# Optimization experiments

Measured on AMD Instinct MI355X. Metric: run time of the kernel, lower is better.

Reference implementation:

```python
import jax, jax.numpy as jnp
import numpy as np

V_MIN = -10.0
V_MAX = 10.0
NUM_ATOMS = 251
B = 131072
N_OBS = 128
N_ACT = 32
HID = 512


def _ln(x, g, b, eps=1e-5):
    m = jnp.mean(x, axis=-1, keepdims=True)
    v = jnp.var(x, axis=-1, keepdims=True)
    return (x - m) * jax.lax.rsqrt(v + eps) * g + b


def setup_inputs() -> dict:
    key = jax.random.key(0)
    ks = jax.random.split(key, 16)

    def lin(k, fi, fo):
        kw, kb = jax.random.split(k)
        lim = 1.0 / np.sqrt(fi)
        W = jax.random.uniform(kw, (fi, fo), jnp.float32, -lim, lim)
        b = jax.random.uniform(kb, (fo,), jnp.float32, -lim, lim)
        return W, b

    W1, b1 = lin(ks[0], N_OBS + N_ACT, HID)
    W2, b2 = lin(ks[1], HID, HID // 2)
    W3, b3 = lin(ks[2], HID // 2, HID // 4)
    W4, b4 = lin(ks[3], HID // 4, NUM_ATOMS)

    return {
        "obs": jax.random.normal(ks[4], (B, N_OBS), jnp.float32),
        "actions": jax.random.normal(ks[5], (B, N_ACT), jnp.float32),
        "rewards": jax.random.normal(ks[6], (B,), jnp.float32),
        "bootstrap": (jax.random.uniform(ks[7], (B,)) > 0.05).astype(jnp.float32),
        "discount": jnp.full((B,), 0.99, jnp.float32),
        "q_support": jnp.linspace(V_MIN, V_MAX, NUM_ATOMS, dtype=jnp.float32),
        "W1": W1, "b1": b1, "g1": jnp.ones((HID,), jnp.float32), "be1": jnp.zeros((HID,), jnp.float32),
        "W2": W2, "b2": b2, "g2": jnp.ones((HID // 2,), jnp.float32), "be2": jnp.zeros((HID // 2,), jnp.float32),
        "W3": W3, "b3": b3, "g3": jnp.ones((HID // 4,), jnp.float32), "be3": jnp.zeros((HID // 4,), jnp.float32),
        "W4": W4, "b4": b4,
    }


def _net(obs, actions, W1, b1, g1, be1, W2, b2, g2, be2, W3, b3, g3, be3, W4, b4):
    x = jnp.concatenate([obs, actions], axis=1)
    x = jax.nn.silu(_ln(x @ W1 + b1, g1, be1))
    x = jax.nn.silu(_ln(x @ W2 + b2, g2, be2))
    x = jax.nn.silu(_ln(x @ W3 + b3, g3, be3))
    return x @ W4 + b4  # [B, NUM_ATOMS] logits


def reference(obs, actions, rewards, bootstrap, discount, q_support,
              W1, b1, g1, be1, W2, b2, g2, be2, W3, b3, g3, be3, W4, b4):
    # C51 categorical projection (DistributionalQNetwork.projection)
    delta_z = (V_MAX - V_MIN) / (NUM_ATOMS - 1)
    bsz = rewards.shape[0]
    target_z = rewards[:, None] + bootstrap[:, None] * discount[:, None] * q_support[None, :]
    target_z = jnp.clip(target_z, V_MIN, V_MAX)
    b = (target_z - V_MIN) / delta_z  # fractional bin positions [B, A]
    lower = jnp.floor(b).astype(jnp.int32)
    upper = jnp.ceil(b).astype(jnp.int32)
    is_integer = upper == lower
    lower_mask = (lower > 0) & is_integer
    upper_mask = (lower == 0) & is_integer
    lower = jnp.where(lower_mask, lower - 1, lower)
    upper = jnp.where(upper_mask, upper + 1, upper)

    logits = _net(obs, actions, W1, b1, g1, be1, W2, b2, g2, be2, W3, b3, g3, be3, W4, b4)
    next_dist = jax.nn.softmax(logits, axis=1)

    offset = (jnp.arange(bsz, dtype=jnp.int32) * NUM_ATOMS)[:, None]  # [B,1]
    max_index = bsz * NUM_ATOMS - 1
    li = jnp.clip((lower + offset).reshape(-1), 0, max_index)
    ui = jnp.clip((upper + offset).reshape(-1), 0, max_index)

    w_lo = (next_dist * (upper.astype(jnp.float32) - b)).reshape(-1)
    w_hi = (next_dist * (b - lower.astype(jnp.float32))).reshape(-1)

    proj = jnp.zeros((bsz * NUM_ATOMS,), next_dist.dtype)
    proj = proj.at[li].add(w_lo).at[ui].add(w_hi)
    return proj.reshape(bsz, NUM_ATOMS)
```

## Files before the change

### kernel.cpp

```cpp
#include <hip/hip_runtime.h>


#define THREADS 256
#define PREP_THREADS 256

typedef __attribute__((ext_vector_type(8))) short short8v;
typedef __attribute__((ext_vector_type(4))) float f32x4;

__device__ __forceinline__ unsigned short f2bf(float f) {
  union { float f; unsigned u; } v; v.f = f;
  unsigned u = v.u;
  u += 0x7fffu + ((u >> 16) & 1u);
  return (unsigned short)(u >> 16);
}
__device__ __forceinline__ unsigned pack2bf(float a, float b) {
  return (unsigned)f2bf(a) | ((unsigned)f2bf(b) << 16);
}

__global__ void prep_kernel(const float* __restrict__ W1, const float* __restrict__ W2,
                            const float* __restrict__ W3, const float* __restrict__ W4,
                            unsigned short* __restrict__ ws) {
  int i = blockIdx.x * PREP_THREADS + threadIdx.x;
  if (i < 81920) {
    int n = i / 160, k = i - n * 160;
    ws[i] = f2bf(W1[k * 512 + n]);
  } else if (i < 212992) {
    int j = i - 81920; int n = j >> 9, k = j & 511;
    ws[i] = f2bf(W2[k * 256 + n]);
  } else if (i < 245760) {
    int j = i - 212992; int n = j >> 8, k = j & 255;
    ws[i] = f2bf(W3[k * 128 + n]);
  } else if (i < 278528) {
    int j = i - 245760; int n = j >> 7, k = j & 127;
    ws[i] = (n < 251) ? f2bf(W4[k * 251 + n]) : (unsigned short)0;
  }
}

#define OFF_R   0
#define OFF_ZS  32768
#define OFF_B4  33792
#define OFF_RED 34816
#define LDS_TOTAL 36096

template<int KD, int NFT>
__device__ __forceinline__ void gemm_w(const unsigned short* __restrict__ WT,
                                       const unsigned char* __restrict__ Hb,
                                       int fbase, f32x4 (&acc)[NFT][2]) {
  const int lane = threadIdx.x & 63;
  const int lm = lane & 15, kg = lane >> 4;
  constexpr int KS  = KD / 32;
  constexpr int G   = (NFT > 4) ? 2 : 1;
  constexpr int FPG = NFT / G;
  constexpr int NIT = KS * G;

  int woff[NFT];
#pragma unroll
  for (int ft = 0; ft < NFT; ++ft)
    woff[ft] = (fbase + ft * 16 + lm) * KD + kg * 8;

  int boff[2][2];
#pragma unroll
  for (int rt = 0; rt < 2; ++rt) {
    const int r = rt * 16 + lm;
    const int swz = (r & 7) << 4;
    const int base = r * (KD * 2) + kg * 16;
    boff[rt][0] = base ^ swz;
    boff[rt][1] = (base + 64) ^ swz;
  }

  short8v abuf[2][FPG];
  short8v bbuf[2][2];
#pragma unroll
  for (int rt = 0; rt < 2; ++rt)
    bbuf[0][rt] = *(const short8v*)(Hb + boff[rt][0]);
#pragma unroll
  for (int f = 0; f < FPG; ++f)
    abuf[0][f] = *(const short8v*)(WT + woff[f]);

#pragma unroll
  for (int it = 0; it < NIT; ++it) {
    const int ks = it / G, g = it % G;
    const int cur = it & 1, nxt = cur ^ 1;
    if (it + 1 < NIT) {
      const int nit = it + 1;
      const int nks = nit / G, ng = nit % G;
      if (ng == 0) {
        const int koff = (nks >> 1) * 128;
#pragma unroll
        for (int rt = 0; rt < 2; ++rt)
          bbuf[nks & 1][rt] = *(const short8v*)(Hb + boff[rt][nks & 1] + koff);
      }
#pragma unroll
      for (int f = 0; f < FPG; ++f)
        abuf[nxt][f] = *(const short8v*)(WT + woff[ng * FPG + f] + nks * 32);
    }
#pragma unroll
    for (int f = 0; f < FPG; ++f) {
      const int ft = g * FPG + f;
      acc[ft][0] = __builtin_amdgcn_mfma_f32_16x16x32_bf16(abuf[cur][f], bbuf[ks & 1][0], acc[ft][0], 0, 0, 0);
      acc[ft][1] = __builtin_amdgcn_mfma_f32_16x16x32_bf16(abuf[cur][f], bbuf[ks & 1][1], acc[ft][1], 0, 0, 0);
    }
  }
}

template<int ND, int NFT>
__device__ __forceinline__ void ln_silu_store(
    f32x4 (&acc)[NFT][2],
    const float* __restrict__ bias, const float* __restrict__ g,
    const float* __restrict__ be, unsigned char* __restrict__ Hb,
    float* __restrict__ redL, int fbase, int fq)
{
  const int lane = threadIdx.x & 63;
  const int lm = lane & 15, kg = lane >> 4;
  float s[2] = {0.f, 0.f}, q[2] = {0.f, 0.f};
#pragma unroll
  for (int ft = 0; ft < NFT; ++ft) {
    const int f0 = fbase + ft * 16 + kg * 4;
    const f32x4 bb = *(const f32x4*)(bias + f0);
#pragma unroll
    for (int rt = 0; rt < 2; ++rt)
#pragma unroll
      for (int rg = 0; rg < 4; ++rg) {
        float x = acc[ft][rt][rg] + bb[rg];
        acc[ft][rt][rg] = x;
        s[rt] += x; q[rt] += x * x;
      }
  }
#pragma unroll
  for (int rt = 0; rt < 2; ++rt) {
    s[rt] += __shfl_xor(s[rt], 16); s[rt] += __shfl_xor(s[rt], 32);
    q[rt] += __shfl_xor(q[rt], 16); q[rt] += __shfl_xor(q[rt], 32);
  }
  if (lane < 16) {
#pragma unroll
    for (int rt = 0; rt < 2; ++rt) {
      redL[(rt * 16 + lm) * 9 + fq * 2    ] = s[rt];
      redL[(rt * 16 + lm) * 9 + fq * 2 + 1] = q[rt];
    }
  }
  __syncthreads();
  float mean[2], rstd[2];
#pragma unroll
  for (int rt = 0; rt < 2; ++rt) {
    const int row = rt * 16 + lm;
    float S = 0.f, Q = 0.f;
#pragma unroll
    for (int w = 0; w < 4; ++w) {
      S += redL[row * 9 + w * 2];
      Q += redL[row * 9 + w * 2 + 1];
    }
    float m = S * (1.0f / ND);
    float v = Q * (1.0f / ND) - m * m;
    mean[rt] = m; rstd[rt] = rsqrtf(v + 1e-5f);
  }
#pragma unroll
  for (int ft = 0; ft < NFT; ++ft) {
    const int f0 = fbase + ft * 16 + kg * 4;
    const f32x4 g4 = *(const f32x4*)(g + f0);
    const f32x4 e4 = *(const f32x4*)(be + f0);
#pragma unroll
    for (int rt = 0; rt < 2; ++rt) {
      const int row = rt * 16 + lm;
      float h[4];
#pragma unroll
      for (int rg = 0; rg < 4; ++rg) {
        float y = (acc[ft][rt][rg] - mean[rt]) * rstd[rt] * g4[rg] + e4[rg];
        h[rg] = y * (1.0f / (1.0f + __expf(-y)));
      }
      uint2 w; w.x = pack2bf(h[0], h[1]); w.y = pack2bf(h[2], h[3]);
      int byte = row * (ND * 2) + f0 * 2;
      byte ^= ((row & 7) << 4);
      *(uint2*)(Hb + byte) = w;
    }
  }
}

__global__ __launch_bounds__(THREADS, 4) void fused_kernel(
    const float* __restrict__ obs, const float* __restrict__ actions,
    const float* __restrict__ rewards, const float* __restrict__ bootstrap,
    const float* __restrict__ discount, const float* __restrict__ q_support,
    const float* __restrict__ b1, const float* __restrict__ g1, const float* __restrict__ be1,
    const float* __restrict__ b2, const float* __restrict__ g2, const float* __restrict__ be2,
    const float* __restrict__ b3, const float* __restrict__ g3, const float* __restrict__ be3,
    const float* __restrict__ b4,
    const unsigned short* __restrict__ ws,
    float* __restrict__ out)
{
  __shared__ __align__(16) unsigned char smem[LDS_TOTAL];
  const int tid  = threadIdx.x;
  const int fq   = tid >> 6;
  const int lane = tid & 63;
  const int lm   = lane & 15;
  const int kg   = lane >> 4;
  const int row0 = blockIdx.x * 32;

  const unsigned short* W1T = ws;
  const unsigned short* W2T = ws + 81920;
  const unsigned short* W3T = ws + 212992;
  const unsigned short* W4T = ws + 245760;

  float* zsL  = (float*)(smem + OFF_ZS);
  float* b4L  = (float*)(smem + OFF_B4);
  float* redL = (float*)(smem + OFF_RED);

  float rw[2], bt[2], dc[2];
#pragma unroll
  for (int rt = 0; rt < 2; ++rt) {
    const int r = row0 + rt * 16 + lm;
    rw[rt] = rewards[r]; bt[rt] = bootstrap[r]; dc[rt] = discount[r];
  }

  zsL[tid] = (tid < 251) ? q_support[tid] : 0.f;
  b4L[tid] = (tid < 251) ? b4[tid] : 0.f;

  {
    unsigned char* Xb = smem + OFF_R;
#pragma unroll
    for (int it = 0; it < 5; ++it) {
      const int qq = it * THREADS + tid;
      const int r  = qq / 40;
      const int c4 = (qq - r * 40) * 4;
      float4 v;
      if (c4 < 128) v = *(const float4*)(obs + (size_t)(row0 + r) * 128 + c4);
      else          v = *(const float4*)(actions + (size_t)(row0 + r) * 32 + (c4 - 128));
      uint2 w; w.x = pack2bf(v.x, v.y); w.y = pack2bf(v.z, v.w);
      int byte = r * 320 + c4 * 2;
      byte ^= ((r & 7) << 4);
      *(uint2*)(Xb + byte) = w;
    }
  }
  __syncthreads();

  f32x4 acc1[8][2];
#pragma unroll
  for (int i = 0; i < 8; ++i) { acc1[i][0] = f32x4{0,0,0,0}; acc1[i][1] = f32x4{0,0,0,0}; }
  gemm_w<160, 8>(W1T, smem + OFF_R, fq * 128, acc1);
  ln_silu_store<512, 8>(acc1, b1, g1, be1, smem + OFF_R, redL, fq * 128, fq);
  __syncthreads();

  f32x4 acc2[4][2];
#pragma unroll
  for (int i = 0; i < 4; ++i) { acc2[i][0] = f32x4{0,0,0,0}; acc2[i][1] = f32x4{0,0,0,0}; }
  gemm_w<512, 4>(W2T, smem + OFF_R, fq * 64, acc2);
  ln_silu_store<256, 4>(acc2, b2, g2, be2, smem + OFF_R, redL, fq * 64, fq);
  __syncthreads();

  f32x4 acc3[2][2];
#pragma unroll
  for (int i = 0; i < 2; ++i) { acc3[i][0] = f32x4{0,0,0,0}; acc3[i][1] = f32x4{0,0,0,0}; }
  gemm_w<256, 2>(W3T, smem + OFF_R, fq * 32, acc3);
  ln_silu_store<128, 2>(acc3, b3, g3, be3, smem + OFF_R, redL, fq * 32, fq);
  __syncthreads();

  f32x4 acc4[4][2];
#pragma unroll
  for (int i = 0; i < 4; ++i) { acc4[i][0] = f32x4{0,0,0,0}; acc4[i][1] = f32x4{0,0,0,0}; }
  gemm_w<128, 4>(W4T, smem + OFF_R, fq * 64, acc4);

  float lv[4][2][4];
#pragma unroll
  for (int ft = 0; ft < 4; ++ft) {
    const int f0 = fq * 64 + ft * 16 + kg * 4;
    const f32x4 bb = *(const f32x4*)(b4L + f0);
#pragma unroll
    for (int rt = 0; rt < 2; ++rt)
#pragma unroll
      for (int rg = 0; rg < 4; ++rg) {
        const int f = f0 + rg;
        lv[ft][rt][rg] = (f < 251) ? (acc4[ft][rt][rg] + bb[rg]) : -1e30f;
      }
  }

#pragma unroll
  for (int rt = 0; rt < 2; ++rt) {
    float m = lv[0][rt][0];
#pragma unroll
    for (int ft = 0; ft < 4; ++ft)
#pragma unroll
      for (int rg = 0; rg < 4; ++rg) m = fmaxf(m, lv[ft][rt][rg]);
    m = fmaxf(m, __shfl_xor(m, 16));
    m = fmaxf(m, __shfl_xor(m, 32));
    if (lane < 16) redL[(rt * 16 + lm) * 5 + fq] = m;
  }
  __syncthreads();

  float* projL = (float*)(smem + OFF_R);
  for (int i = tid; i < 32 * 251; i += THREADS) projL[i] = 0.f;

  float gm[2];
#pragma unroll
  for (int rt = 0; rt < 2; ++rt) {
    const int row = rt * 16 + lm;
    float m = redL[row * 5];
#pragma unroll
    for (int w = 1; w < 4; ++w) m = fmaxf(m, redL[row * 5 + w]);
    gm[rt] = m;
  }
  __syncthreads();
#pragma unroll
  for (int rt = 0; rt < 2; ++rt) {
    float E = 0.f;
#pragma unroll
    for (int ft = 0; ft < 4; ++ft)
#pragma unroll
      for (int rg = 0; rg < 4; ++rg) {
        float e = __expf(lv[ft][rt][rg] - gm[rt]);
        lv[ft][rt][rg] = e;
        E += e;
      }
    E += __shfl_xor(E, 16); E += __shfl_xor(E, 32);
    if (lane < 16) redL[(rt * 16 + lm) * 5 + fq] = E;
  }
  __syncthreads();
  float inv[2];
#pragma unroll
  for (int rt = 0; rt < 2; ++rt) {
    const int row = rt * 16 + lm;
    float E = 0.f;
#pragma unroll
    for (int w = 0; w < 4; ++w) E += redL[row * 5 + w];
    inv[rt] = 1.0f / E;
  }

  constexpr float DZF = 20.0f / 250.0f;
#pragma unroll
  for (int ft = 0; ft < 4; ++ft) {
    const int f0 = fq * 64 + ft * 16 + kg * 4;
    const f32x4 z4 = *(const f32x4*)(zsL + f0);
#pragma unroll
    for (int rt = 0; rt < 2; ++rt) {
      const int base = (rt * 16 + lm) * 251;
      const float bd = __fmul_rn(bt[rt], dc[rt]);
#pragma unroll
      for (int rg = 0; rg < 4; ++rg) {
        const int f = f0 + rg;
        if (f < 251) {
          const float p = lv[ft][rt][rg] * inv[rt];
          float t = __fadd_rn(rw[rt], __fmul_rn(bd, z4[rg]));
          t = fminf(fmaxf(t, -10.0f), 10.0f);
          const float bfr = __fdiv_rn(__fsub_rn(t, -10.0f), DZF);
          const float fl = floorf(bfr), fu = ceilf(bfr);
          int l = (int)fl, u = (int)fu;
          if (fl == fu) { if (l > 0) --l; else ++u; }
          atomicAdd(projL + base + l, p * ((float)u - bfr));
          atomicAdd(projL + base + u, p * (bfr - (float)l));
        }
      }
    }
  }
  __syncthreads();

  const float4* ps = (const float4*)projL;
  float4* po = (float4*)(out + (size_t)row0 * 251);
  for (int i = tid; i < 2008; i += THREADS) po[i] = ps[i];
}

extern "C" void kernel_launch(void* const* d_in, const int* in_sizes, int n_in,
                              void* d_out, int out_size, void* d_ws, size_t ws_size,
                              hipStream_t stream) {
  const float* obs  = (const float*)d_in[0];
  const float* act  = (const float*)d_in[1];
  const float* rew  = (const float*)d_in[2];
  const float* boot = (const float*)d_in[3];
  const float* disc = (const float*)d_in[4];
  const float* zs   = (const float*)d_in[5];
  const float* W1   = (const float*)d_in[6];
  const float* b1   = (const float*)d_in[7];
  const float* g1   = (const float*)d_in[8];
  const float* be1  = (const float*)d_in[9];
  const float* W2   = (const float*)d_in[10];
  const float* b2   = (const float*)d_in[11];
  const float* g2   = (const float*)d_in[12];
  const float* be2  = (const float*)d_in[13];
  const float* W3   = (const float*)d_in[14];
  const float* b3   = (const float*)d_in[15];
  const float* g3   = (const float*)d_in[16];
  const float* be3  = (const float*)d_in[17];
  const float* W4   = (const float*)d_in[18];
  const float* b4   = (const float*)d_in[19];
  unsigned short* wsp = (unsigned short*)d_ws;

  const int Bn = in_sizes[2];
  prep_kernel<<<(278528 + PREP_THREADS - 1) / PREP_THREADS, PREP_THREADS, 0, stream>>>(
      W1, W2, W3, W4, wsp);
  fused_kernel<<<Bn / 32, THREADS, 0, stream>>>(obs, act, rew, boot, disc, zs,
      b1, g1, be1, b2, g2, be2, b3, g3, be3, b4, wsp, (float*)d_out);
}
```

Before: 482.8 us.

## Deepen GEMM prefetch pipeline, use hardware bf16 pack, replace division with multiply

```diff
diff --git a/kernel.cpp b/kernel.cpp
--- a/kernel.cpp
+++ b/kernel.cpp
@@ -14,7 +14,9 @@
   return (unsigned short)(u >> 16);
 }
 __device__ __forceinline__ unsigned pack2bf(float a, float b) {
-  return (unsigned)f2bf(a) | ((unsigned)f2bf(b) << 16);
+  unsigned r;
+  asm("v_cvt_pk_bf16_f32 %0, %1, %2" : "=v"(r) : "v"(a), "v"(b));
+  return r;
 }
 
 __global__ void prep_kernel(const float* __restrict__ W1, const float* __restrict__ W2,
@@ -42,22 +44,19 @@
 #define OFF_RED 34816
 #define LDS_TOTAL 36096
 
-template<int KD, int NFT>
+template<int KD, int NFT, int FPG, int DEPTH>
 __device__ __forceinline__ void gemm_w(const unsigned short* __restrict__ WT,
                                        const unsigned char* __restrict__ Hb,
                                        int fbase, f32x4 (&acc)[NFT][2]) {
   const int lane = threadIdx.x & 63;
   const int lm = lane & 15, kg = lane >> 4;
   constexpr int KS  = KD / 32;
-  constexpr int G   = (NFT > 4) ? 2 : 1;
-  constexpr int FPG = NFT / G;
+  constexpr int G   = NFT / FPG;
   constexpr int NIT = KS * G;
-
-  int woff[NFT];
-#pragma unroll
-  for (int ft = 0; ft < NFT; ++ft)
-    woff[ft] = (fbase + ft * 16 + lm) * KD + kg * 8;
-
+  constexpr int PF  = DEPTH - 1;
+  constexpr int PB  = DEPTH - 1;
+
+  const int woff0 = (fbase + lm) * KD + kg * 8;
   int boff[2][2];
 #pragma unroll
   for (int rt = 0; rt < 2; ++rt) {
@@ -68,37 +67,50 @@
     boff[rt][1] = (base + 64) ^ swz;
   }
 
-  short8v abuf[2][FPG];
-  short8v bbuf[2][2];
-#pragma unroll
-  for (int rt = 0; rt < 2; ++rt)
-    bbuf[0][rt] = *(const short8v*)(Hb + boff[rt][0]);
-#pragma unroll
-  for (int f = 0; f < FPG; ++f)
-    abuf[0][f] = *(const short8v*)(WT + woff[f]);
+  short8v abuf[DEPTH][FPG];
+  short8v bbuf[DEPTH][2];
+
+#pragma unroll
+  for (int ks = 0; ks < PB && ks < KS; ++ks) {
+    const int koff = (ks >> 1) * 128;
+#pragma unroll
+    for (int rt = 0; rt < 2; ++rt)
+      bbuf[ks % DEPTH][rt] = *(const short8v*)(Hb + boff[rt][ks & 1] + koff);
+  }
+#pragma unroll
+  for (int p = 0; p < PF && p < NIT; ++p) {
+    const int g = p % G, ks = p / G;
+#pragma unroll
+    for (int f = 0; f < FPG; ++f)
+      abuf[p % DEPTH][f] =
+          *(const short8v*)(WT + woff0 + (g * FPG + f) * (16 * KD) + ks * 32);
+  }
 
 #pragma unroll
   for (int it = 0; it < NIT; ++it) {
     const int ks = it / G, g = it % G;
-    const int cur = it & 1, nxt = cur ^ 1;
-    if (it + 1 < NIT) {
-      const int nit = it + 1;
-      const int nks = nit / G, ng = nit % G;
-      if (ng == 0) {
-        const int koff = (nks >> 1) * 128;
-#pragma unroll
-        for (int rt = 0; rt < 2; ++rt)
-          bbuf[nks & 1][rt] = *(const short8v*)(Hb + boff[rt][nks & 1] + koff);
-      }
+    if (g == 0 && ks + PB < KS) {
+      const int nks = ks + PB;
+      const int koff = (nks >> 1) * 128;
+#pragma unroll
+      for (int rt = 0; rt < 2; ++rt)
+        bbuf[nks % DEPTH][rt] = *(const short8v*)(Hb + boff[rt][nks & 1] + koff);
+    }
+    if (it + PF < NIT) {
+      const int nit = it + PF;
+      const int ng = nit % G, nks = nit / G;
 #pragma unroll
       for (int f = 0; f < FPG; ++f)
-        abuf[nxt][f] = *(const short8v*)(WT + woff[ng * FPG + f] + nks * 32);
+        abuf[nit % DEPTH][f] =
+            *(const short8v*)(WT + woff0 + (ng * FPG + f) * (16 * KD) + nks * 32);
     }
 #pragma unroll
     for (int f = 0; f < FPG; ++f) {
       const int ft = g * FPG + f;
-      acc[ft][0] = __builtin_amdgcn_mfma_f32_16x16x32_bf16(abuf[cur][f], bbuf[ks & 1][0], acc[ft][0], 0, 0, 0);
-      acc[ft][1] = __builtin_amdgcn_mfma_f32_16x16x32_bf16(abuf[cur][f], bbuf[ks & 1][1], acc[ft][1], 0, 0, 0);
+      acc[ft][0] = __builtin_amdgcn_mfma_f32_16x16x32_bf16(
+          abuf[it % DEPTH][f], bbuf[ks % DEPTH][0], acc[ft][0], 0, 0, 0);
+      acc[ft][1] = __builtin_amdgcn_mfma_f32_16x16x32_bf16(
+          abuf[it % DEPTH][f], bbuf[ks % DEPTH][1], acc[ft][1], 0, 0, 0);
     }
   }
 }
@@ -234,28 +246,28 @@
   f32x4 acc1[8][2];
 #pragma unroll
   for (int i = 0; i < 8; ++i) { acc1[i][0] = f32x4{0,0,0,0}; acc1[i][1] = f32x4{0,0,0,0}; }
-  gemm_w<160, 8>(W1T, smem + OFF_R, fq * 128, acc1);
+  gemm_w<160, 8, 2, 2>(W1T, smem + OFF_R, fq * 128, acc1);
   ln_silu_store<512, 8>(acc1, b1, g1, be1, smem + OFF_R, redL, fq * 128, fq);
   __syncthreads();
 
   f32x4 acc2[4][2];
 #pragma unroll
   for (int i = 0; i < 4; ++i) { acc2[i][0] = f32x4{0,0,0,0}; acc2[i][1] = f32x4{0,0,0,0}; }
-  gemm_w<512, 4>(W2T, smem + OFF_R, fq * 64, acc2);
+  gemm_w<512, 4, 2, 3>(W2T, smem + OFF_R, fq * 64, acc2);
   ln_silu_store<256, 4>(acc2, b2, g2, be2, smem + OFF_R, redL, fq * 64, fq);
   __syncthreads();
 
   f32x4 acc3[2][2];
 #pragma unroll
   for (int i = 0; i < 2; ++i) { acc3[i][0] = f32x4{0,0,0,0}; acc3[i][1] = f32x4{0,0,0,0}; }
-  gemm_w<256, 2>(W3T, smem + OFF_R, fq * 32, acc3);
+  gemm_w<256, 2, 2, 3>(W3T, smem + OFF_R, fq * 32, acc3);
   ln_silu_store<128, 2>(acc3, b3, g3, be3, smem + OFF_R, redL, fq * 32, fq);
   __syncthreads();
 
   f32x4 acc4[4][2];
 #pragma unroll
   for (int i = 0; i < 4; ++i) { acc4[i][0] = f32x4{0,0,0,0}; acc4[i][1] = f32x4{0,0,0,0}; }
-  gemm_w<128, 4>(W4T, smem + OFF_R, fq * 64, acc4);
+  gemm_w<128, 4, 2, 3>(W4T, smem + OFF_R, fq * 64, acc4);
 
   float lv[4][2][4];
 #pragma unroll
@@ -323,6 +335,7 @@
   }
 
   constexpr float DZF = 20.0f / 250.0f;
+  constexpr float INVDZ = 1.0f / DZF;
 #pragma unroll
   for (int ft = 0; ft < 4; ++ft) {
     const int f0 = fq * 64 + ft * 16 + kg * 4;
@@ -338,7 +351,7 @@
           const float p = lv[ft][rt][rg] * inv[rt];
           float t = __fadd_rn(rw[rt], __fmul_rn(bd, z4[rg]));
           t = fminf(fmaxf(t, -10.0f), 10.0f);
-          const float bfr = __fdiv_rn(__fsub_rn(t, -10.0f), DZF);
+          const float bfr = __fmul_rn(__fsub_rn(t, -10.0f), INVDZ);
           const float fl = floorf(bfr), fu = ceilf(bfr);
           int l = (int)fl, u = (int)fu;
           if (fl == fu) { if (l > 0) --l; else ++u; }
```

New measurement: 489.6 us. No clear change (+1.4%).

## Roll GEMM loops, use hardware bf16 pack, replace division with reciprocal multiply

Applied to the files above, without the earlier changes.

```diff
diff --git a/kernel.cpp b/kernel.cpp
--- a/kernel.cpp
+++ b/kernel.cpp
@@ -14,7 +14,9 @@
   return (unsigned short)(u >> 16);
 }
 __device__ __forceinline__ unsigned pack2bf(float a, float b) {
-  return (unsigned)f2bf(a) | ((unsigned)f2bf(b) << 16);
+  unsigned r;
+  asm("v_cvt_pk_bf16_f32 %0, %1, %2" : "=v"(r) : "v"(a), "v"(b));
+  return r;
 }
 
 __global__ void prep_kernel(const float* __restrict__ W1, const float* __restrict__ W2,
@@ -43,63 +45,61 @@
 #define LDS_TOTAL 36096
 
 template<int KD, int NFT>
-__device__ __forceinline__ void gemm_w(const unsigned short* __restrict__ WT,
-                                       const unsigned char* __restrict__ Hb,
-                                       int fbase, f32x4 (&acc)[NFT][2]) {
+__device__ __forceinline__ void gemm_rolled(const unsigned short* __restrict__ WT,
+                                            const unsigned char* __restrict__ Hb,
+                                            int fbase, f32x4 (&acc)[NFT][2]) {
+  constexpr int KS = KD / 32;
   const int lane = threadIdx.x & 63;
   const int lm = lane & 15, kg = lane >> 4;
-  constexpr int KS  = KD / 32;
-  constexpr int G   = (NFT > 4) ? 2 : 1;
-  constexpr int FPG = NFT / G;
-  constexpr int NIT = KS * G;
-
-  int woff[NFT];
-#pragma unroll
-  for (int ft = 0; ft < NFT; ++ft)
-    woff[ft] = (fbase + ft * 16 + lm) * KD + kg * 8;
-
-  int boff[2][2];
+  const unsigned short* wp = WT + (fbase + lm) * KD + kg * 8;
+  int bbase[2], bswz[2];
 #pragma unroll
   for (int rt = 0; rt < 2; ++rt) {
     const int r = rt * 16 + lm;
-    const int swz = (r & 7) << 4;
-    const int base = r * (KD * 2) + kg * 16;
-    boff[rt][0] = base ^ swz;
-    boff[rt][1] = (base + 64) ^ swz;
-  }
-
-  short8v abuf[2][FPG];
-  short8v bbuf[2][2];
-#pragma unroll
-  for (int rt = 0; rt < 2; ++rt)
-    bbuf[0][rt] = *(const short8v*)(Hb + boff[rt][0]);
-#pragma unroll
-  for (int f = 0; f < FPG; ++f)
-    abuf[0][f] = *(const short8v*)(WT + woff[f]);
-
-#pragma unroll
-  for (int it = 0; it < NIT; ++it) {
-    const int ks = it / G, g = it % G;
-    const int cur = it & 1, nxt = cur ^ 1;
-    if (it + 1 < NIT) {
-      const int nit = it + 1;
-      const int nks = nit / G, ng = nit % G;
-      if (ng == 0) {
-        const int koff = (nks >> 1) * 128;
-#pragma unroll
-        for (int rt = 0; rt < 2; ++rt)
-          bbuf[nks & 1][rt] = *(const short8v*)(Hb + boff[rt][nks & 1] + koff);
-      }
-#pragma unroll
-      for (int f = 0; f < FPG; ++f)
-        abuf[nxt][f] = *(const short8v*)(WT + woff[ng * FPG + f] + nks * 32);
-    }
-#pragma unroll
-    for (int f = 0; f < FPG; ++f) {
-      const int ft = g * FPG + f;
-      acc[ft][0] = __builtin_amdgcn_mfma_f32_16x16x32_bf16(abuf[cur][f], bbuf[ks & 1][0], acc[ft][0], 0, 0, 0);
-      acc[ft][1] = __builtin_amdgcn_mfma_f32_16x16x32_bf16(abuf[cur][f], bbuf[ks & 1][1], acc[ft][1], 0, 0, 0);
-    }
+    bbase[rt] = r * (KD * 2) + kg * 16;
+    bswz[rt] = (r & 7) << 4;
+  }
+  short8v A0[NFT], A1[NFT], B0[2], B1[2];
+
+  auto loadA = [&](short8v (&A)[NFT], int k) {
+#pragma unroll
+    for (int ft = 0; ft < NFT; ++ft)
+      A[ft] = *(const short8v*)(wp + ft * (16 * KD) + k * 32);
+  };
+  auto loadB = [&](short8v (&B)[2], int k) {
+#pragma unroll
+    for (int rt = 0; rt < 2; ++rt)
+      B[rt] = *(const short8v*)(Hb + ((bbase[rt] + k * 64) ^ bswz[rt]));
+  };
+  auto domfma = [&](short8v (&A)[NFT], short8v (&B)[2]) {
+#pragma unroll
+    for (int ft = 0; ft < NFT; ++ft) {
+      acc[ft][0] = __builtin_amdgcn_mfma_f32_16x16x32_bf16(A[ft], B[0], acc[ft][0], 0, 0, 0);
+      acc[ft][1] = __builtin_amdgcn_mfma_f32_16x16x32_bf16(A[ft], B[1], acc[ft][1], 0, 0, 0);
+    }
+  };
+
+  loadA(A0, 0); loadB(B0, 0);
+  if constexpr ((KS & 1) == 0) {
+#pragma unroll 1
+    for (int ks = 0; ks < KS - 2; ks += 2) {
+      loadA(A1, ks + 1); loadB(B1, ks + 1);
+      domfma(A0, B0);
+      loadA(A0, ks + 2); loadB(B0, ks + 2);
+      domfma(A1, B1);
+    }
+    loadA(A1, KS - 1); loadB(B1, KS - 1);
+    domfma(A0, B0);
+    domfma(A1, B1);
+  } else {
+#pragma unroll 1
+    for (int ks = 0; ks < KS - 1; ks += 2) {
+      loadA(A1, ks + 1); loadB(B1, ks + 1);
+      domfma(A0, B0);
+      loadA(A0, ks + 2); loadB(B0, ks + 2);
+      domfma(A1, B1);
+    }
+    domfma(A0, B0);
   }
 }
 
@@ -215,7 +215,7 @@
 
   {
     unsigned char* Xb = smem + OFF_R;
-#pragma unroll
+#pragma unroll 1
     for (int it = 0; it < 5; ++it) {
       const int qq = it * THREADS + tid;
       const int r  = qq / 40;
@@ -234,28 +234,28 @@
   f32x4 acc1[8][2];
 #pragma unroll
   for (int i = 0; i < 8; ++i) { acc1[i][0] = f32x4{0,0,0,0}; acc1[i][1] = f32x4{0,0,0,0}; }
-  gemm_w<160, 8>(W1T, smem + OFF_R, fq * 128, acc1);
+  gemm_rolled<160, 8>(W1T, smem + OFF_R, fq * 128, acc1);
   ln_silu_store<512, 8>(acc1, b1, g1, be1, smem + OFF_R, redL, fq * 128, fq);
   __syncthreads();
 
   f32x4 acc2[4][2];
 #pragma unroll
   for (int i = 0; i < 4; ++i) { acc2[i][0] = f32x4{0,0,0,0}; acc2[i][1] = f32x4{0,0,0,0}; }
-  gemm_w<512, 4>(W2T, smem + OFF_R, fq * 64, acc2);
+  gemm_rolled<512, 4>(W2T, smem + OFF_R, fq * 64, acc2);
   ln_silu_store<256, 4>(acc2, b2, g2, be2, smem + OFF_R, redL, fq * 64, fq);
   __syncthreads();
 
   f32x4 acc3[2][2];
 #pragma unroll
   for (int i = 0; i < 2; ++i) { acc3[i][0] = f32x4{0,0,0,0}; acc3[i][1] = f32x4{0,0,0,0}; }
-  gemm_w<256, 2>(W3T, smem + OFF_R, fq * 32, acc3);
+  gemm_rolled<256, 2>(W3T, smem + OFF_R, fq * 32, acc3);
   ln_silu_store<128, 2>(acc3, b3, g3, be3, smem + OFF_R, redL, fq * 32, fq);
   __syncthreads();
 
   f32x4 acc4[4][2];
 #pragma unroll
   for (int i = 0; i < 4; ++i) { acc4[i][0] = f32x4{0,0,0,0}; acc4[i][1] = f32x4{0,0,0,0}; }
-  gemm_w<128, 4>(W4T, smem + OFF_R, fq * 64, acc4);
+  gemm_rolled<128, 4>(W4T, smem + OFF_R, fq * 64, acc4);
 
   float lv[4][2][4];
 #pragma unroll
@@ -323,6 +323,7 @@
   }
 
   constexpr float DZF = 20.0f / 250.0f;
+  constexpr float INVDZ = 1.0f / DZF;
 #pragma unroll
   for (int ft = 0; ft < 4; ++ft) {
     const int f0 = fq * 64 + ft * 16 + kg * 4;
@@ -338,7 +339,7 @@
           const float p = lv[ft][rt][rg] * inv[rt];
           float t = __fadd_rn(rw[rt], __fmul_rn(bd, z4[rg]));
           t = fminf(fmaxf(t, -10.0f), 10.0f);
-          const float bfr = __fdiv_rn(__fsub_rn(t, -10.0f), DZF);
+          const float bfr = __fmul_rn(__fsub_rn(t, -10.0f), INVDZ);
           const float fl = floorf(bfr), fu = ceilf(bfr);
           int l = (int)fl, u = (int)fu;
           if (fl == fu) { if (l > 0) --l; else ++u; }
```

New measurement: 483.1 us. About the same (+0.0%).
